# Kernel optimization log

Measured on AMD Instinct MI355X. Metric: run time of the kernel, lower is better.

The kernel has to match this reference:

```python
import jax, jax.numpy as jnp
import numpy as np
import math

MAXL = 3
TAUS = [16, 16, 16, 16]
OUT_TAUS = [16, 16, 16, 16]
BM_CNT = 1.0
BM_EPS = 1e-5

# (l1, l2, l) triples in the kernel's triple-loop order, bucketed by output l
TRIPLES = {l: [] for l in range(MAXL + 1)}
for _l1 in range(MAXL + 1):
    for _l2 in range(_l1 + 1):
        for _l in range(_l1 - _l2, min(_l1 + _l2, MAXL) + 1):
            TRIPLES[_l].append((_l1, _l2))

MIDDLE_TAUS = [sum(TAUS[a] * TAUS[b] for (a, b) in TRIPLES[l]) for l in range(MAXL + 1)]


def _cg_coef(l1, m1, l2, m2, l, m):
    if m1 + m2 != m:
        return 0.0
    f = math.factorial
    pre = math.sqrt((2 * l + 1) * f(l1 + l2 - l) * f(l1 - l2 + l) * f(-l1 + l2 + l) / f(l1 + l2 + l + 1))
    pre *= math.sqrt(f(l + m) * f(l - m) * f(l1 - m1) * f(l1 + m1) * f(l2 - m2) * f(l2 + m2))
    s = 0.0
    for k in range(0, l1 + l2 - l + 1):
        d = [k, l1 + l2 - l - k, l1 - m1 - k, l2 + m2 - k, l - l2 + m1 + k, l - l1 - m2 + k]
        if any(x < 0 for x in d):
            continue
        den = 1.0
        for x in d:
            den *= f(x)
        s += (-1.0) ** k / den
    return pre * s


def _cg_tensor(l1, l2, l):
    t = np.zeros((2 * l1 + 1, 2 * l2 + 1, 2 * l + 1), dtype=np.float32)
    for i, m1 in enumerate(range(-l1, l1 + 1)):
        for j, m2 in enumerate(range(-l2, l2 + 1)):
            m = m1 + m2
            if -l <= m <= l:
                t[i, j, m + l] = _cg_coef(l1, m1, l2, m2, l, m)
    return t

CG = {}
for _l in range(MAXL + 1):
    for (_l1, _l2) in TRIPLES[_l]:
        CG[(_l1, _l2, _l)] = jnp.asarray(_cg_tensor(_l1, _l2, _l))

# complex-multiply contraction tensor: (a*b)[k] = a[i] b[j] CM[i,j,k]
_CM = np.zeros((2, 2, 2), dtype=np.float32)
_CM[0, 0, 0] = 1.0; _CM[1, 1, 0] = -1.0; _CM[0, 1, 1] = 1.0; _CM[1, 0, 1] = 1.0
CM = jnp.asarray(_CM)


def setup_inputs() -> dict:
    key = jax.random.key(0)
    k1, k2, k3 = jax.random.split(key, 3)
    in_len = sum(TAUS[l] * (2 * l + 1) for l in range(MAXL + 1))  # 256
    wlen = sum(OUT_TAUS[l] * MIDDLE_TAUS[l] for l in range(MAXL + 1))  # 90112
    activations = jax.random.normal(k1, (2048, in_len, 2), dtype=jnp.float32)
    W = 0.05 * jax.random.uniform(k2, (wlen, 2), dtype=jnp.float32)
    bn_stds = jax.random.uniform(k3, (sum(MIDDLE_TAUS),), dtype=jnp.float32)
    return {"activations": activations, "W": W, "bn_stds": bn_stds}


def reference(activations, W, bn_stds):
    B = activations.shape[0]
    # split input into per-l parts: [B, tau_l, 2l+1, 2]
    Fs = []
    st = 0
    for l in range(MAXL + 1):
        ln = TAUS[l] * (2 * l + 1)
        Fs.append(activations[:, st:st + ln, :].reshape(B, TAUS[l], 2 * l + 1, 2))
        st += ln
    outs = []
    w_st = 0
    s_st = 0
    for l in range(MAXL + 1):
        # Clebsch-Gordan products feeding output degree l
        mids = []
        for (l1, l2) in TRIPLES[l]:
            c = jnp.einsum('btmi,bsnj,mnp,ijk->btspk', Fs[l1], Fs[l2], CG[(l1, l2, l)], CM)
            mids.append(c.reshape(B, TAUS[l1] * TAUS[l2], 2 * l + 1, 2))
        mid = jnp.concatenate(mids, axis=1)  # [B, M_l, 2l+1, 2]
        Ml = MIDDLE_TAUS[l]
        # fused batchnorm: per-middle-channel std over batch and m, moving average update
        batch_std = jnp.sqrt(jnp.mean(jnp.sum(mid * mid, axis=-1), axis=(0, 2)))  # [M_l]
        mov = bn_stds[s_st:s_st + Ml]
        new_std = (mov * BM_CNT + batch_std) / (BM_CNT + 1.0)
        mid = mid / (new_std + BM_EPS)[None, :, None, None]
        # complex linear mix over middle channels -> out_taus[l]
        wl = jax.lax.dynamic_slice_in_dim(W, w_st, OUT_TAUS[l] * Ml, axis=0).reshape(OUT_TAUS[l], Ml, 2)
        out_l = jnp.einsum('oci,bcmj,ijk->bomk', wl, mid, CM)
        outs.append(out_l.reshape(B, OUT_TAUS[l] * (2 * l + 1), 2))
        w_st += OUT_TAUS[l] * Ml
        s_st += Ml
    return jnp.concatenate(outs, axis=1)  # [B, 256, 2]
```

## Files before the change

kernel.cpp:

```cpp
#include <hip/hip_runtime.h>
#include <math.h>

typedef __attribute__((ext_vector_type(8))) short bf16x8;
typedef __attribute__((ext_vector_type(4))) float f32x4;

constexpr double cfact(int n){ double r=1.0; for(int i=2;i<=n;++i) r*=(double)i; return r; }
constexpr double csqrt_(double x){ double g=(x>1.0)?x:1.0; for(int i=0;i<100;++i) g=0.5*(g+x/g); return g; }
constexpr double cg_coef_(int l1,int m1,int l2,int m2,int l,int m){
  double pre = csqrt_((double)(2*l+1)*cfact(l1+l2-l)*cfact(l1-l2+l)*cfact(-l1+l2+l)/cfact(l1+l2+l+1));
  pre = pre*csqrt_(cfact(l+m)*cfact(l-m)*cfact(l1-m1)*cfact(l1+m1)*cfact(l2-m2)*cfact(l2+m2));
  double s=0.0;
  for(int k=0;k<=l1+l2-l;++k){
    int d0=k,d1=l1+l2-l-k,d2=l1-m1-k,d3=l2+m2-k,d4=l-l2+m1+k,d5=l-l1-m2+k;
    if(d0<0||d1<0||d2<0||d3<0||d4<0||d5<0) continue;
    double den=cfact(d0)*cfact(d1)*cfact(d2)*cfact(d3)*cfact(d4)*cfact(d5);
    s+=((k&1)?-1.0:1.0)/den;
  }
  return pre*s;
}
struct CGList{ int n; float coef[64]; int mi[64]; int ni[64]; int pi[64]; };
constexpr CGList build_cg(int l1,int l2,int l){
  CGList T{};
  for(int i=0;i<2*l1+1;++i){
    for(int j=0;j<2*l2+1;++j){
      int m1=i-l1, m2=j-l2, m=m1+m2;
      if(m<-l||m>l) continue;
      double c=cg_coef_(l1,m1,l2,m2,l,m);
      if(c>1e-12||c<-1e-12){
        T.coef[T.n]=(float)c; T.mi[T.n]=i; T.ni[T.n]=j; T.pi[T.n]=m+l; T.n++;
      }
    }
  }
  return T;
}

__device__ __host__ constexpr int AOFF(int l){ return l==0?0: l==1?16: l==2?64:144; }
__device__ __host__ constexpr int MLs(int l){ return l==0?1024: l==1?1536: l==2?1792:1536; }
__device__ __host__ constexpr int WOFF(int l){ return l==0?0: l==1?16384: l==2?40960:69632; }
__device__ __host__ constexpr int SOFF(int l){ return l==0?0: l==1?1024: l==2?2560:4352; }
__device__ __host__ constexpr int ABASE(int l){ return l==0?0: l==1?65536: l==2?163840:278528; }

#define DEVFN __device__ __forceinline__
#define BP 68
#define AP 68

DEVFN unsigned f2bf2(float x, float y){
  unsigned ux = __float_as_uint(x); ux = (ux + 0x7FFFu + ((ux>>16)&1u)) >> 16;
  unsigned uy = __float_as_uint(y); uy = (uy + 0x7FFFu + ((uy>>16)&1u)) >> 16;
  return (ux & 0xFFFFu) | (uy << 16);
}

template<int L1,int L2,int L>
DEVFN void cg_accum(const float2* F1, const float2* F2, float2* mid){
  constexpr CGList T = build_cg(L1,L2,L);
  #pragma unroll
  for(int e=0;e<T.n;++e){
    const float c = T.coef[e];
    const float2 a = F1[T.mi[e]];
    const float2 b = F2[T.ni[e]];
    float pr = a.x*b.x - a.y*b.y;
    float pim= a.x*b.y + a.y*b.x;
    mid[T.pi[e]].x += c*pr;
    mid[T.pi[e]].y += c*pim;
  }
}

template<int L1,int L2,int L>
DEVFN void k1g(const float2* __restrict__ act2, int b0, int u, int bh,
               float& ssa, float& ssb){
  constexpr int N1=2*L1+1, N2=2*L2+1, NP=2*L+1;
  const int t = u>>3, s0 = (u&7)*2;
  const float2* base1  = act2 + AOFF(L1) + t*N1;
  const float2* base2a = act2 + AOFF(L2) + s0*N2;
  const float2* base2b = base2a + N2;
  #pragma unroll 2
  for(int bi=0;bi<16;++bi){
    const size_t ro = (size_t)(b0 + bh*16 + bi)*256;
    float2 F1[N1], F2a[N2], F2b[N2], mida[NP], midb[NP];
    #pragma unroll
    for(int m=0;m<N1;++m) F1[m]=base1[ro+m];
    #pragma unroll
    for(int n=0;n<N2;++n){ F2a[n]=base2a[ro+n]; F2b[n]=base2b[ro+n]; }
    #pragma unroll
    for(int p=0;p<NP;++p){ mida[p]=make_float2(0.f,0.f); midb[p]=make_float2(0.f,0.f); }
    cg_accum<L1,L2,L>(F1,F2a,mida);
    cg_accum<L1,L2,L>(F1,F2b,midb);
    #pragma unroll
    for(int p=0;p<NP;++p){
      ssa += mida[p].x*mida[p].x + mida[p].y*mida[p].y;
      ssb += midb[p].x*midb[p].x + midb[p].y*midb[p].y;
    }
  }
}

DEVFN void convW(const float* __restrict__ W, short* __restrict__ A, int idx){
  int l = (idx<1024)?0 : (idx<2560)?1 : (idx<4352)?2 : 3;
  int c = idx - SOFF(l);
  int Ml = MLs(l);
  const float2* wbase = (const float2*)W + WOFF(l) + c;
  unsigned* Aw = (unsigned*)(A + ABASE(l));
  #pragma unroll 4
  for(int o=0;o<16;++o){
    float2 w = wbase[(size_t)o*Ml];
    Aw[(size_t)o*Ml + c]      = f2bf2(w.x, -w.y);
    Aw[(size_t)(o+16)*Ml + c] = f2bf2(w.y,  w.x);
  }
}

__global__ __launch_bounds__(256) void k_sumsq(const float* __restrict__ act,
                                               float2* __restrict__ part,
                                               const float* __restrict__ W,
                                               short* __restrict__ A){
  const int bid = blockIdx.x;
  const int tid = threadIdx.x;
  if(bid >= 1472){
    convW(W, A, (bid-1472)*256 + tid);
    return;
  }
  const int order[23] = {22,16,21,18,15,20,13,9,14,8,17,7,12,6,10,3,5,19,2,11,1,4,0};
  const int ti = order[bid>>6];
  const int chunk = bid&63;
  const int b0 = chunk*32;
  const int u = tid & 127, bh = tid >> 7;
  const float2* act2 = (const float2*)act;
  float ssa=0.f, ssb=0.f;
  switch(ti){
    case 0:  k1g<0,0,0>(act2,b0,u,bh,ssa,ssb); break;
    case 1:  k1g<1,1,0>(act2,b0,u,bh,ssa,ssb); break;
    case 2:  k1g<2,2,0>(act2,b0,u,bh,ssa,ssb); break;
    case 3:  k1g<3,3,0>(act2,b0,u,bh,ssa,ssb); break;
    case 4:  k1g<1,0,1>(act2,b0,u,bh,ssa,ssb); break;
    case 5:  k1g<1,1,1>(act2,b0,u,bh,ssa,ssb); break;
    case 6:  k1g<2,1,1>(act2,b0,u,bh,ssa,ssb); break;
    case 7:  k1g<2,2,1>(act2,b0,u,bh,ssa,ssb); break;
    case 8:  k1g<3,2,1>(act2,b0,u,bh,ssa,ssb); break;
    case 9:  k1g<3,3,1>(act2,b0,u,bh,ssa,ssb); break;
    case 10: k1g<1,1,2>(act2,b0,u,bh,ssa,ssb); break;
    case 11: k1g<2,0,2>(act2,b0,u,bh,ssa,ssb); break;
    case 12: k1g<2,1,2>(act2,b0,u,bh,ssa,ssb); break;
    case 13: k1g<2,2,2>(act2,b0,u,bh,ssa,ssb); break;
    case 14: k1g<3,1,2>(act2,b0,u,bh,ssa,ssb); break;
    case 15: k1g<3,2,2>(act2,b0,u,bh,ssa,ssb); break;
    case 16: k1g<3,3,2>(act2,b0,u,bh,ssa,ssb); break;
    case 17: k1g<2,1,3>(act2,b0,u,bh,ssa,ssb); break;
    case 18: k1g<2,2,3>(act2,b0,u,bh,ssa,ssb); break;
    case 19: k1g<3,0,3>(act2,b0,u,bh,ssa,ssb); break;
    case 20: k1g<3,1,3>(act2,b0,u,bh,ssa,ssb); break;
    case 21: k1g<3,2,3>(act2,b0,u,bh,ssa,ssb); break;
    default: k1g<3,3,3>(act2,b0,u,bh,ssa,ssb); break;
  }
  part[(size_t)((ti*64 + chunk)*2 + bh)*128 + u] = make_float2(ssa, ssb);
}

__global__ __launch_bounds__(256) void k_scale(const float* __restrict__ bn,
                                               const float2* __restrict__ part,
                                               float* __restrict__ s){
  const int ti = blockIdx.x;
  const int ch = threadIdx.x;
  const int idx = ti*256 + ch;
  const int u = ch>>1;
  const float2* ps = part + (size_t)ti*128*128 + u;
  float sum = 0.f;
  #pragma unroll 8
  for(int r=0;r<128;++r){
    float2 v = ps[(size_t)r*128];
    sum += (ch&1) ? v.y : v.x;
  }
  int l = (idx<1024)?0 : (idx<2560)?1 : (idx<4352)?2 : 3;
  float divi = (l==0)?(1.f/2048.f) : (l==1)?(1.f/6144.f) : (l==2)?(1.f/10240.f) : (1.f/14336.f);
  float bstd = sqrtf(sum*divi);
  float nstd = 0.5f*(bn[idx]+bstd);
  s[idx] = 1.f/(nstd+1e-5f);
}


#define SA_B   0
#define BT_B   16384
#define LA_B   33792

template<int NTIL>
DEVFN void kf_pre(const float* __restrict__ act, char* smem, int b0){
  const int tid = threadIdx.x;
  const float2* actg2 = (const float2*)act + (size_t)b0*256;
  float4* s4 = (float4*)(smem + SA_B);
  const float4* ag = (const float4*)actg2;
  #pragma unroll
  for(int j=0;j<4;++j) s4[j*256+tid] = ag[j*256+tid];
  unsigned* btile = (unsigned*)(smem + BT_B);
  for(int i=tid; i<NTIL*16*BP; i+=256) btile[i]=0;
  __syncthreads();
}

template<int L1,int L2,int L,int Q,int NTIL>
DEVFN void kf_triple(char* smem, const unsigned* __restrict__ Aw,
                     const float* __restrict__ sg, f32x4& cR, f32x4& cI){
  constexpr int N1=2*L1+1, N2=2*L2+1, NP=2*L+1;
  constexpr int Ml = MLs(L);
  const float2* sa = (const float2*)(smem + SA_B);
  unsigned* btile  = (unsigned*)(smem + BT_B);
  unsigned* ldsA   = (unsigned*)(smem + LA_B);
  const int tid = threadIdx.x;
  const int lane = tid & 63, w = tid >> 6;
  const int col = lane & 15, quad = lane >> 4;
  const int up = tid & 31, bi = tid >> 5;
  const int r0 = tid>>4,       j0 = (tid&15)*4;
  const int r1 = (tid+256)>>4;
  {
    const int base = (Q*4)*64;
    uint4 v0 = *(const uint4*)(Aw + (size_t)r0*Ml + base + j0);
    uint4 v1 = *(const uint4*)(Aw + (size_t)r1*Ml + base + j0);
    *(uint4*)(ldsA + r0*AP + j0) = v0;
    *(uint4*)(ldsA + r1*AP + j0) = v1;
  }
  #pragma unroll 1
  for(int cc=0; cc<4; ++cc){
    unsigned* cbuf = ldsA + (cc&1)*(32*AP);
    unsigned* nbuf = ldsA + ((cc+1)&1)*(32*AP);
    uint4 v0, v1;
    if(cc<3){
      const int base = (Q*4+cc+1)*64;
      v0 = *(const uint4*)(Aw + (size_t)r0*Ml + base + j0);
      v1 = *(const uint4*)(Aw + (size_t)r1*Ml + base + j0);
    }
    {
      const float2 s2 = *(const float2*)(sg + SOFF(L) + Q*256 + cc*64 + 2*up);
      const int u = cc*32 + up;
      const int t = u>>3, s0 = (u&7)*2;
      const float2* arow = sa + bi*256;
      float2 F1[N1], F2a[N2], F2b[N2], mida[NP], midb[NP];
      #pragma unroll
      for(int m=0;m<N1;++m) F1[m]=arow[AOFF(L1)+t*N1+m];
      #pragma unroll
      for(int n=0;n<N2;++n){
        F2a[n]=arow[AOFF(L2)+s0*N2+n];
        F2b[n]=arow[AOFF(L2)+(s0+1)*N2+n];
      }
      #pragma unroll
      for(int p=0;p<NP;++p){ mida[p]=make_float2(0.f,0.f); midb[p]=make_float2(0.f,0.f); }
      cg_accum<L1,L2,L>(F1,F2a,mida);
      cg_accum<L1,L2,L>(F1,F2b,midb);
      #pragma unroll
      for(int p=0;p<NP;++p){
        uint2 v;
        v.x = f2bf2(mida[p].x*s2.x, mida[p].y*s2.x);
        v.y = f2bf2(midb[p].x*s2.y, midb[p].y*s2.y);
        *(uint2*)(btile + (size_t)(bi*NP+p)*BP + 2*up) = v;
      }
    }
    if(cc<3){
      *(uint4*)(nbuf + r0*AP + j0) = v0;
      *(uint4*)(nbuf + r1*AP + j0) = v1;
    }
    __syncthreads();
    if(w < NTIL){
      const unsigned* ar0 = cbuf + col*AP + quad*4;
      const unsigned* ar1 = cbuf + (col+16)*AP + quad*4;
      const unsigned* bb  = btile + (w*16+col)*BP + quad*4;
      #pragma unroll
      for(int ks=0; ks<4; ++ks){
        bf16x8 b  = *(const bf16x8*)(bb + ks*16);
        bf16x8 A0 = *(const bf16x8*)(ar0 + ks*16);
        bf16x8 A1 = *(const bf16x8*)(ar1 + ks*16);
        cR = __builtin_amdgcn_mfma_f32_16x16x32_bf16(A0, b, cR, 0, 0, 0);
        cI = __builtin_amdgcn_mfma_f32_16x16x32_bf16(A1, b, cI, 0, 0, 0);
      }
    }
    __syncthreads();
  }
}

template<int L,int NTIL>
DEVFN void kf_epi(float* __restrict__ out, int b0, f32x4 cR, f32x4 cI){
  constexpr int NP = 2*L+1;
  const int tid = threadIdx.x, lane = tid & 63, w = tid >> 6;
  const int col = lane & 15, quad = lane >> 4;
  if(w < NTIL){
    const int r = w*16 + col;
    if(r < 8*NP){
      const int b = b0 + r/NP, p = r - (r/NP)*NP;
      float2* o2 = (float2*)out + (size_t)b*256 + AOFF(L);
      #pragma unroll
      for(int i=0;i<4;++i) o2[(quad*4+i)*NP + p] = make_float2(cR[i], cI[i]);
    }
  }
}

__global__ __launch_bounds__(256,3) void k_fusedall(const float* __restrict__ act,
    const short* __restrict__ A, const float* __restrict__ sg,
    float* __restrict__ out){
  __shared__ __align__(16) char smem[51200];
  const int bid = blockIdx.x;
  f32x4 cR={0.f,0.f,0.f,0.f}, cI={0.f,0.f,0.f,0.f};
  if(bid < 256){
    const int b0 = bid*8;
    kf_pre<4>(act,smem,b0);
    const unsigned* Aw=(const unsigned*)(A+ABASE(3));
    kf_triple<2,1,3,0,4>(smem,Aw,sg,cR,cI);
    kf_triple<2,2,3,1,4>(smem,Aw,sg,cR,cI);
    kf_triple<3,0,3,2,4>(smem,Aw,sg,cR,cI);
    kf_triple<3,1,3,3,4>(smem,Aw,sg,cR,cI);
    kf_triple<3,2,3,4,4>(smem,Aw,sg,cR,cI);
    kf_triple<3,3,3,5,4>(smem,Aw,sg,cR,cI);
    kf_epi<3,4>(out,b0,cR,cI);
  } else if(bid < 512){
    const int b0 = (bid-256)*8;
    kf_pre<3>(act,smem,b0);
    const unsigned* Aw=(const unsigned*)(A+ABASE(2));
    kf_triple<1,1,2,0,3>(smem,Aw,sg,cR,cI);
    kf_triple<2,0,2,1,3>(smem,Aw,sg,cR,cI);
    kf_triple<2,1,2,2,3>(smem,Aw,sg,cR,cI);
    kf_triple<2,2,2,3,3>(smem,Aw,sg,cR,cI);
    kf_triple<3,1,2,4,3>(smem,Aw,sg,cR,cI);
    kf_triple<3,2,2,5,3>(smem,Aw,sg,cR,cI);
    kf_triple<3,3,2,6,3>(smem,Aw,sg,cR,cI);
    kf_epi<2,3>(out,b0,cR,cI);
  } else if(bid < 768){
    const int b0 = (bid-512)*8;
    kf_pre<2>(act,smem,b0);
    const unsigned* Aw=(const unsigned*)(A+ABASE(1));
    kf_triple<1,0,1,0,2>(smem,Aw,sg,cR,cI);
    kf_triple<1,1,1,1,2>(smem,Aw,sg,cR,cI);
    kf_triple<2,1,1,2,2>(smem,Aw,sg,cR,cI);
    kf_triple<2,2,1,3,2>(smem,Aw,sg,cR,cI);
    kf_triple<3,2,1,4,2>(smem,Aw,sg,cR,cI);
    kf_triple<3,3,1,5,2>(smem,Aw,sg,cR,cI);
    kf_epi<1,2>(out,b0,cR,cI);
  } else {
    const int b0 = (bid-768)*8;
    kf_pre<1>(act,smem,b0);
    const unsigned* Aw=(const unsigned*)(A+ABASE(0));
    kf_triple<0,0,0,0,1>(smem,Aw,sg,cR,cI);
    kf_triple<1,1,0,1,1>(smem,Aw,sg,cR,cI);
    kf_triple<2,2,0,2,1>(smem,Aw,sg,cR,cI);
    kf_triple<3,3,0,3,1>(smem,Aw,sg,cR,cI);
    kf_epi<0,1>(out,b0,cR,cI);
  }
}

extern "C" void kernel_launch(void* const* d_in, const int* in_sizes, int n_in,
                              void* d_out, int out_size, void* d_ws, size_t ws_size,
                              hipStream_t stream) {
  const float* act = (const float*)d_in[0];
  const float* W   = (const float*)d_in[1];
  const float* bn  = (const float*)d_in[2];
  float* out = (float*)d_out;

  float*  s    = (float*)d_ws;
  short*  A    = (short*)((char*)d_ws + 24576);
  float2* part = (float2*)((char*)d_ws + 1048576);

  hipLaunchKernelGGL(k_sumsq,   dim3(1495), dim3(256), 0, stream, act, part, W, A);
  hipLaunchKernelGGL(k_scale,   dim3(23),   dim3(256), 0, stream, bn, part, s);
  hipLaunchKernelGGL(k_fusedall,dim3(1024), dim3(256), 0, stream, act, A, s, out);
}
```

Baseline: 143.0 us.

## Drop LDS activation staging and A double-buffer to cut shared memory

Activations are now read straight from global memory, through the cache, inside each triple instead of being staged in LDS. The weight tile uses a single LDS buffer with register prefetch in place of double buffering. Shared memory per block falls from about 50KB to about 26KB, and launch bounds rise from 3 to 4 blocks per CU to allow higher occupancy. The cost is repeated global or L1 loads of activations, and a single-buffered A tile that is written before the barrier, which could reduce overlap.

```diff
diff --git a/kernel.cpp b/kernel.cpp
--- a/kernel.cpp
+++ b/kernel.cpp
@@ -174,29 +174,23 @@
 }
 
 
-#define SA_B   0
-#define BT_B   16384
-#define LA_B   33792
+#define BT_B   0
+#define LA_B   17408
 
 template<int NTIL>
-DEVFN void kf_pre(const float* __restrict__ act, char* smem, int b0){
+DEVFN void kf_pre(char* smem){
   const int tid = threadIdx.x;
-  const float2* actg2 = (const float2*)act + (size_t)b0*256;
-  float4* s4 = (float4*)(smem + SA_B);
-  const float4* ag = (const float4*)actg2;
-  #pragma unroll
-  for(int j=0;j<4;++j) s4[j*256+tid] = ag[j*256+tid];
   unsigned* btile = (unsigned*)(smem + BT_B);
   for(int i=tid; i<NTIL*16*BP; i+=256) btile[i]=0;
   __syncthreads();
 }
 
 template<int L1,int L2,int L,int Q,int NTIL>
-DEVFN void kf_triple(char* smem, const unsigned* __restrict__ Aw,
+DEVFN void kf_triple(const float2* __restrict__ act2, int b0, char* smem,
+                     const unsigned* __restrict__ Aw,
                      const float* __restrict__ sg, f32x4& cR, f32x4& cI){
   constexpr int N1=2*L1+1, N2=2*L2+1, NP=2*L+1;
   constexpr int Ml = MLs(L);
-  const float2* sa = (const float2*)(smem + SA_B);
   unsigned* btile  = (unsigned*)(smem + BT_B);
   unsigned* ldsA   = (unsigned*)(smem + LA_B);
   const int tid = threadIdx.x;
@@ -205,28 +199,15 @@
   const int up = tid & 31, bi = tid >> 5;
   const int r0 = tid>>4,       j0 = (tid&15)*4;
   const int r1 = (tid+256)>>4;
-  {
-    const int base = (Q*4)*64;
-    uint4 v0 = *(const uint4*)(Aw + (size_t)r0*Ml + base + j0);
-    uint4 v1 = *(const uint4*)(Aw + (size_t)r1*Ml + base + j0);
-    *(uint4*)(ldsA + r0*AP + j0) = v0;
-    *(uint4*)(ldsA + r1*AP + j0) = v1;
-  }
+  const float2* arow = act2 + (size_t)(b0+bi)*256;
+  uint4 v0 = *(const uint4*)(Aw + (size_t)r0*Ml + Q*256 + j0);
+  uint4 v1 = *(const uint4*)(Aw + (size_t)r1*Ml + Q*256 + j0);
   #pragma unroll 1
   for(int cc=0; cc<4; ++cc){
-    unsigned* cbuf = ldsA + (cc&1)*(32*AP);
-    unsigned* nbuf = ldsA + ((cc+1)&1)*(32*AP);
-    uint4 v0, v1;
-    if(cc<3){
-      const int base = (Q*4+cc+1)*64;
-      v0 = *(const uint4*)(Aw + (size_t)r0*Ml + base + j0);
-      v1 = *(const uint4*)(Aw + (size_t)r1*Ml + base + j0);
-    }
     {
       const float2 s2 = *(const float2*)(sg + SOFF(L) + Q*256 + cc*64 + 2*up);
       const int u = cc*32 + up;
       const int t = u>>3, s0 = (u&7)*2;
-      const float2* arow = sa + bi*256;
       float2 F1[N1], F2a[N2], F2b[N2], mida[NP], midb[NP];
       #pragma unroll
       for(int m=0;m<N1;++m) F1[m]=arow[AOFF(L1)+t*N1+m];
@@ -247,14 +228,17 @@
         *(uint2*)(btile + (size_t)(bi*NP+p)*BP + 2*up) = v;
       }
     }
+    *(uint4*)(ldsA + r0*AP + j0) = v0;
+    *(uint4*)(ldsA + r1*AP + j0) = v1;
     if(cc<3){
-      *(uint4*)(nbuf + r0*AP + j0) = v0;
-      *(uint4*)(nbuf + r1*AP + j0) = v1;
+      const int base = Q*256 + (cc+1)*64;
+      v0 = *(const uint4*)(Aw + (size_t)r0*Ml + base + j0);
+      v1 = *(const uint4*)(Aw + (size_t)r1*Ml + base + j0);
     }
     __syncthreads();
     if(w < NTIL){
-      const unsigned* ar0 = cbuf + col*AP + quad*4;
-      const unsigned* ar1 = cbuf + (col+16)*AP + quad*4;
+      const unsigned* ar0 = ldsA + col*AP + quad*4;
+      const unsigned* ar1 = ldsA + (col+16)*AP + quad*4;
       const unsigned* bb  = btile + (w*16+col)*BP + quad*4;
       #pragma unroll
       for(int ks=0; ks<4; ++ks){
@@ -285,54 +269,55 @@
   }
 }
 
-__global__ __launch_bounds__(256,3) void k_fusedall(const float* __restrict__ act,
+__global__ __launch_bounds__(256,4) void k_fusedall(const float* __restrict__ act,
     const short* __restrict__ A, const float* __restrict__ sg,
     float* __restrict__ out){
-  __shared__ __align__(16) char smem[51200];
+  __shared__ __align__(16) char smem[26112];
   const int bid = blockIdx.x;
+  const float2* act2 = (const float2*)act;
   f32x4 cR={0.f,0.f,0.f,0.f}, cI={0.f,0.f,0.f,0.f};
   if(bid < 256){
     const int b0 = bid*8;
-    kf_pre<4>(act,smem,b0);
+    kf_pre<4>(smem);
     const unsigned* Aw=(const unsigned*)(A+ABASE(3));
-    kf_triple<2,1,3,0,4>(smem,Aw,sg,cR,cI);
-    kf_triple<2,2,3,1,4>(smem,Aw,sg,cR,cI);
-    kf_triple<3,0,3,2,4>(smem,Aw,sg,cR,cI);
-    kf_triple<3,1,3,3,4>(smem,Aw,sg,cR,cI);
-    kf_triple<3,2,3,4,4>(smem,Aw,sg,cR,cI);
-    kf_triple<3,3,3,5,4>(smem,Aw,sg,cR,cI);
+    kf_triple<2,1,3,0,4>(act2,b0,smem,Aw,sg,cR,cI);
+    kf_triple<2,2,3,1,4>(act2,b0,smem,Aw,sg,cR,cI);
+    kf_triple<3,0,3,2,4>(act2,b0,smem,Aw,sg,cR,cI);
+    kf_triple<3,1,3,3,4>(act2,b0,smem,Aw,sg,cR,cI);
+    kf_triple<3,2,3,4,4>(act2,b0,smem,Aw,sg,cR,cI);
+    kf_triple<3,3,3,5,4>(act2,b0,smem,Aw,sg,cR,cI);
     kf_epi<3,4>(out,b0,cR,cI);
   } else if(bid < 512){
     const int b0 = (bid-256)*8;
-    kf_pre<3>(act,smem,b0);
+    kf_pre<3>(smem);
     const unsigned* Aw=(const unsigned*)(A+ABASE(2));
-    kf_triple<1,1,2,0,3>(smem,Aw,sg,cR,cI);
-    kf_triple<2,0,2,1,3>(smem,Aw,sg,cR,cI);
-    kf_triple<2,1,2,2,3>(smem,Aw,sg,cR,cI);
-    kf_triple<2,2,2,3,3>(smem,Aw,sg,cR,cI);
-    kf_triple<3,1,2,4,3>(smem,Aw,sg,cR,cI);
-    kf_triple<3,2,2,5,3>(smem,Aw,sg,cR,cI);
-    kf_triple<3,3,2,6,3>(smem,Aw,sg,cR,cI);
+    kf_triple<1,1,2,0,3>(act2,b0,smem,Aw,sg,cR,cI);
+    kf_triple<2,0,2,1,3>(act2,b0,smem,Aw,sg,cR,cI);
+    kf_triple<2,1,2,2,3>(act2,b0,smem,Aw,sg,cR,cI);
+    kf_triple<2,2,2,3,3>(act2,b0,smem,Aw,sg,cR,cI);
+    kf_triple<3,1,2,4,3>(act2,b0,smem,Aw,sg,cR,cI);
+    kf_triple<3,2,2,5,3>(act2,b0,smem,Aw,sg,cR,cI);
+    kf_triple<3,3,2,6,3>(act2,b0,smem,Aw,sg,cR,cI);
     kf_epi<2,3>(out,b0,cR,cI);
   } else if(bid < 768){
     const int b0 = (bid-512)*8;
-    kf_pre<2>(act,smem,b0);
+    kf_pre<2>(smem);
     const unsigned* Aw=(const unsigned*)(A+ABASE(1));
-    kf_triple<1,0,1,0,2>(smem,Aw,sg,cR,cI);
-    kf_triple<1,1,1,1,2>(smem,Aw,sg,cR,cI);
-    kf_triple<2,1,1,2,2>(smem,Aw,sg,cR,cI);
-    kf_triple<2,2,1,3,2>(smem,Aw,sg,cR,cI);
-    kf_triple<3,2,1,4,2>(smem,Aw,sg,cR,cI);
-    kf_triple<3,3,1,5,2>(smem,Aw,sg,cR,cI);
+    kf_triple<1,0,1,0,2>(act2,b0,smem,Aw,sg,cR,cI);
+    kf_triple<1,1,1,1,2>(act2,b0,smem,Aw,sg,cR,cI);
+    kf_triple<2,1,1,2,2>(act2,b0,smem,Aw,sg,cR,cI);
+    kf_triple<2,2,1,3,2>(act2,b0,smem,Aw,sg,cR,cI);
+    kf_triple<3,2,1,4,2>(act2,b0,smem,Aw,sg,cR,cI);
+    kf_triple<3,3,1,5,2>(act2,b0,smem,Aw,sg,cR,cI);
     kf_epi<1,2>(out,b0,cR,cI);
   } else {
     const int b0 = (bid-768)*8;
-    kf_pre<1>(act,smem,b0);
+    kf_pre<1>(smem);
     const unsigned* Aw=(const unsigned*)(A+ABASE(0));
-    kf_triple<0,0,0,0,1>(smem,Aw,sg,cR,cI);
-    kf_triple<1,1,0,1,1>(smem,Aw,sg,cR,cI);
-    kf_triple<2,2,0,2,1>(smem,Aw,sg,cR,cI);
-    kf_triple<3,3,0,3,1>(smem,Aw,sg,cR,cI);
+    kf_triple<0,0,0,0,1>(act2,b0,smem,Aw,sg,cR,cI);
+    kf_triple<1,1,0,1,1>(act2,b0,smem,Aw,sg,cR,cI);
+    kf_triple<2,2,0,2,1>(act2,b0,smem,Aw,sg,cR,cI);
+    kf_triple<3,3,0,3,1>(act2,b0,smem,Aw,sg,cR,cI);
     kf_epi<0,1>(out,b0,cR,cI);
   }
 }
```

After: 153.9 us. 1.08x slower.
